# Kernel optimization log

Measured on AMD Instinct MI355X. Metric: run time of the kernel, lower is better.

Reference implementation:

```python
import jax, jax.numpy as jnp
import numpy as np

DIM, DEPTH, HEADS, DIM_HEAD, MLP = 768, 6, 12, 64, 3072
INNER = HEADS * DIM_HEAD
B, N = 8, 1024
SCALE = DIM_HEAD ** -0.5
EPS = 1e-5


def _ln(x, g, b):
    m = jnp.mean(x, -1, keepdims=True)
    v = jnp.mean(jnp.square(x - m), -1, keepdims=True)
    return (x - m) * jax.lax.rsqrt(v + EPS) * g + b


def _ternary(w):
    # BitNet-style ternary quant with straight-through estimator
    s = jnp.mean(jnp.abs(w)) + 1e-8
    wq = jnp.clip(jnp.round(w / s), -1.0, 1.0) * s
    return w + jax.lax.stop_gradient(wq - w)


def setup_inputs() -> dict:
    key = jax.random.key(0)
    ks = jax.random.split(key, 8)
    d = {
        'x': jax.random.normal(ks[0], (B, N, DIM), jnp.float32),
        'ln1_g': jnp.ones((DEPTH, DIM), jnp.float32),
        'ln1_b': jnp.zeros((DEPTH, DIM), jnp.float32),
        'Wqkv': jax.random.normal(ks[1], (DEPTH, 3 * INNER, DIM), jnp.float32) * 0.02,
        'ln2_g': jnp.ones((DEPTH, INNER), jnp.float32),
        'ln2_b': jnp.zeros((DEPTH, INNER), jnp.float32),
        'Wo': jax.random.normal(ks[2], (DEPTH, DIM, INNER), jnp.float32) * 0.02,
        'bo': jnp.zeros((DEPTH, DIM), jnp.float32),
        'ffln1_g': jnp.ones((DEPTH, DIM), jnp.float32),
        'ffln1_b': jnp.zeros((DEPTH, DIM), jnp.float32),
        'W1': jax.random.normal(ks[3], (DEPTH, MLP, DIM), jnp.float32) * 0.02,
        'b1': jnp.zeros((DEPTH, MLP), jnp.float32),
        'ffln2_g': jnp.ones((DEPTH, MLP), jnp.float32),
        'ffln2_b': jnp.zeros((DEPTH, MLP), jnp.float32),
        'W2': jax.random.normal(ks[4], (DEPTH, DIM, MLP), jnp.float32) * 0.02,
        'b2': jnp.zeros((DEPTH, DIM), jnp.float32),
    }
    return d


def _forward(x, ln1_g, ln1_b, Wqkv, ln2_g, ln2_b, Wo, bo,
             ffln1_g, ffln1_b, W1, b1, ffln2_g, ffln2_b, W2, b2):
    depth = Wqkv.shape[0]
    # layers 0..depth-2 ternary, last layer plain linear
    flag = jnp.concatenate([jnp.ones((depth - 1,), x.dtype), jnp.zeros((1,), x.dtype)])

    def block(h, p):
        (g1, b1n, wqkv, g2, b2n, wo, bo_, fg1, fb1, w1, bb1, fg2, fb2, w2, bb2, f) = p

        def mt(w):
            return f * _ternary(w) + (1.0 - f) * w

        y = _ln(h, g1, b1n)
        qkv = jnp.einsum('bnd,ed->bne', y, mt(wqkv))  # [B,N,3*INNER]
        q, k, v = jnp.split(qkv, 3, axis=-1)
        def heads(t):
            return t.reshape(B, N, HEADS, DIM_HEAD).transpose(0, 2, 1, 3)
        q, k, v = heads(q), heads(k), heads(v)
        attn = jax.nn.softmax(jnp.einsum('bhnd,bhmd->bhnm', q, k) * SCALE, axis=-1)
        o = jnp.einsum('bhnm,bhmd->bhnd', attn, v)
        o = o.transpose(0, 2, 1, 3).reshape(B, N, INNER)
        o = _ln(o, g2, b2n)
        o = jnp.einsum('bne,de->bnd', o, mt(wo)) + bo_
        h = h + o
        y = _ln(h, fg1, fb1)
        y = jnp.einsum('bnd,md->bnm', y, mt(w1)) + bb1
        y = jax.nn.gelu(y, approximate=False)
        y = _ln(y, fg2, fb2)
        y = jnp.einsum('bnm,dm->bnd', y, mt(w2)) + bb2
        return h + y, None

    xs = (ln1_g, ln1_b, Wqkv, ln2_g, ln2_b, Wo, bo,
          ffln1_g, ffln1_b, W1, b1, ffln2_g, ffln2_b, W2, b2, flag)
    out, _ = jax.lax.scan(block, x, xs)
    return out


def reference(x, ln1_g, ln1_b, Wqkv, ln2_g, ln2_b, Wo, bo,
              ffln1_g, ffln1_b, W1, b1, ffln2_g, ffln2_b, W2, b2):
    return _forward(x, ln1_g, ln1_b, Wqkv, ln2_g, ln2_b, Wo, bo,
                    ffln1_g, ffln1_b, W1, b1, ffln2_g, ffln2_b, W2, b2)
```

## Files before the change

kernel.cpp:

```cpp
#include <hip/hip_runtime.h>
#include <hip/hip_bf16.h>
#include <math.h>

typedef __bf16 bf16_t;
typedef __bf16 bf16x4 __attribute__((ext_vector_type(4)));
typedef __bf16 bf16x8 __attribute__((ext_vector_type(8)));
typedef float  f32x4  __attribute__((ext_vector_type(4)));

#define TOKENS 8192
#define DIMV   768
#define INNERV 768
#define QKVW   2304
#define MLPW   3072
#define NSEQ   1024
#define NB     8
#define NH     12
#define DH     64

enum { EP_STORE = 0, EP_BIAS_RES = 1, EP_BIAS_GELU = 2 };

__device__ __forceinline__ void gload_lds16(const bf16_t* g, bf16_t* l)
{
  __builtin_amdgcn_global_load_lds((const __attribute__((address_space(1))) void*)g,
                                   (__attribute__((address_space(3))) void*)l,
                                   16, 0, 0);
}

__device__ __forceinline__ float gelu_fast(float x)
{
  const float z = fabsf(x) * 0.70710678118654752f;
  const float d = fmaf(0.3275911f, z, 1.0f);
#if __has_builtin(__builtin_amdgcn_rcpf)
  const float t = __builtin_amdgcn_rcpf(d);
#else
  const float t = 1.0f / d;
#endif
  float p = fmaf(t, 1.061405429f, -1.453152027f);
  p = fmaf(t, p, 1.421413741f);
  p = fmaf(t, p, -0.284496736f);
  p = fmaf(t, p, 0.254829592f);
  p = t * p;
  const float e = __expf(-z * z);
  float erfv = fmaf(-p, e, 1.0f);
  erfv = copysignf(erfv, x);
  return 0.5f * x * (1.0f + erfv);
}

template <int BM>
__global__ __launch_bounds__(256)
void gemm_nt(const bf16_t* __restrict__ A, const bf16_t* __restrict__ B,
             const int K, const int N, const int mode,
             const float* __restrict__ sacc_p, const float sinvn, const float sbias,
             const float* __restrict__ bias,
             float* __restrict__ resid,
             bf16_t* __restrict__ outb,
             float* __restrict__ fout)
{
  constexpr int MI = BM / 32;
  constexpr int WR = BM / 2;
  __shared__ __align__(16) bf16_t lsA[2][BM * 32];
  __shared__ __align__(16) bf16_t lsB[2][128 * 32];
  const int tid  = threadIdx.x;
  const int lane = tid & 63;
  const int wave = tid >> 6;
  const int wm = wave >> 1, wn = wave & 1;
  const int bm = blockIdx.x, bn = blockIdx.y;

  const int srB   = wave * 32 + (lane >> 2);
  const int fswB  = (srB >> 1) & 3;
  const int scolB = ((lane & 3) ^ fswB) * 8;
  const bf16_t* gB = B + (size_t)(bn * 128 + srB) * K + scolB;
  const int lb0 = srB * 32 + (lane & 3) * 8;
  const int lb1 = (srB + 16) * 32 + (lane & 3) * 8;

  const int srA   = (BM == 128) ? srB : (wave * 16 + (lane >> 2));
  const int fswA  = (srA >> 1) & 3;
  const int scolA = ((lane & 3) ^ fswA) * 8;
  const bf16_t* gA = A + (size_t)(bm * BM + srA) * K + scolA;
  const int la0 = srA * 32 + (lane & 3) * 8;
  const int la1 = (srA + 16) * 32 + (lane & 3) * 8;

  f32x4 acc[MI][4];
#pragma unroll
  for (int i = 0; i < MI; i++)
#pragma unroll
    for (int j = 0; j < 4; j++) acc[i][j] = (f32x4){0.f, 0.f, 0.f, 0.f};

  const int fr   = ((lane & 15) >> 1) & 3;
  const int rsl  = ((lane >> 4) ^ fr) * 8;
  const int arow = (wm * WR + (lane & 15)) * 32 + rsl;
  const int brow = (wn * 64 + (lane & 15)) * 32 + rsl;

  auto stage = [&](int b, int kb) {
    gload_lds16(gA + kb, &lsA[b][la0]);
    if constexpr (BM == 128) gload_lds16(gA + (size_t)16 * K + kb, &lsA[b][la1]);
    gload_lds16(gB + kb, &lsB[b][lb0]);
    gload_lds16(gB + (size_t)16 * K + kb, &lsB[b][lb1]);
  };
  auto compute = [&](int b) {
    bf16x8 af[MI], bfv[4];
#pragma unroll
    for (int i = 0; i < MI; i++) af[i]  = *(const bf16x8*)&lsA[b][arow + i * 16 * 32];
#pragma unroll
    for (int j = 0; j < 4; j++)  bfv[j] = *(const bf16x8*)&lsB[b][brow + j * 16 * 32];
#pragma unroll
    for (int i = 0; i < MI; i++)
#pragma unroll
      for (int j = 0; j < 4; j++)
        acc[i][j] = __builtin_amdgcn_mfma_f32_16x16x32_bf16(af[i], bfv[j], acc[i][j], 0, 0, 0);
  };

  const int NT = K / 32;
  stage(0, 0);
  stage(1, 32);
  int cur = 0;
  for (int t = 0; t < NT - 1; ++t) {
    if constexpr (BM == 128) asm volatile("s_waitcnt vmcnt(4)" ::: "memory");
    else                     asm volatile("s_waitcnt vmcnt(3)" ::: "memory");
    __builtin_amdgcn_s_barrier();
    __builtin_amdgcn_sched_barrier(0);
    compute(cur);
    asm volatile("s_waitcnt lgkmcnt(0)" ::: "memory");
    __builtin_amdgcn_s_barrier();
    __builtin_amdgcn_sched_barrier(0);
    if (t + 2 < NT) stage(cur, (t + 2) * 32);
    cur ^= 1;
  }
  asm volatile("s_waitcnt vmcnt(0)" ::: "memory");
  __builtin_amdgcn_s_barrier();
  __builtin_amdgcn_sched_barrier(0);
  compute(cur);

  const float s = (*sacc_p) * sinvn + sbias;
  const int r0 = bm * BM + wm * WR + (lane >> 4) * 4;
  const int c0 = bn * 128 + wn * 64 + (lane & 15);
#pragma unroll
  for (int i = 0; i < MI; i++) {
#pragma unroll
    for (int j = 0; j < 4; j++) {
      const int col = c0 + j * 16;
#pragma unroll
      for (int r = 0; r < 4; r++) {
        const int row = r0 + i * 16 + r;
        const float v = acc[i][j][r] * s;
        const size_t idx = (size_t)row * N + col;
        if (mode == EP_STORE) {
          outb[idx] = (bf16_t)v;
        } else if (mode == EP_BIAS_RES) {
          const float add = v + bias[col];
          if (fout) fout[idx] = resid[idx] + add;
          else      resid[idx] += add;
        } else {
          outb[idx] = (bf16_t)gelu_fast(v + bias[col]);
        }
      }
    }
  }
}

template <typename TIN>
__global__ __launch_bounds__(256)
void ln_kern(const TIN* __restrict__ x, const float* __restrict__ g,
             const float* __restrict__ b, bf16_t* __restrict__ y, const int W)
{
  const int row = blockIdx.x;
  const int tid = threadIdx.x;
  const TIN* xr = x + (size_t)row * W;
  float s = 0.f, s2 = 0.f;
  if constexpr (sizeof(TIN) == 4) {
    const f32x4* xv = (const f32x4*)xr;
    for (int i = tid; i < W / 4; i += 256) {
      f32x4 v = xv[i];
#pragma unroll
      for (int e = 0; e < 4; e++) { s += v[e]; s2 += v[e] * v[e]; }
    }
  } else {
    const bf16x8* xv = (const bf16x8*)xr;
    for (int i = tid; i < W / 8; i += 256) {
      bf16x8 v = xv[i];
#pragma unroll
      for (int e = 0; e < 8; e++) { const float f = (float)v[e]; s += f; s2 += f * f; }
    }
  }
#pragma unroll
  for (int off = 32; off > 0; off >>= 1) {
    s  += __shfl_xor(s,  off, 64);
    s2 += __shfl_xor(s2, off, 64);
  }
  __shared__ float red[8];
  if ((tid & 63) == 0) { red[(tid >> 6) * 2] = s; red[(tid >> 6) * 2 + 1] = s2; }
  __syncthreads();
  const float ts  = red[0] + red[2] + red[4] + red[6];
  const float ts2 = red[1] + red[3] + red[5] + red[7];
  const float invW = 1.0f / (float)W;
  const float mean = ts * invW;
  const float var  = fmaxf(ts2 * invW - mean * mean, 0.f);
  const float rs   = rsqrtf(var + 1e-5f);
  bf16_t* yr = y + (size_t)row * W;
  const f32x4* gv = (const f32x4*)g;
  const f32x4* bv = (const f32x4*)b;
  if constexpr (sizeof(TIN) == 4) {
    const f32x4* xv = (const f32x4*)xr;
    bf16x4* yv = (bf16x4*)yr;
    for (int i = tid; i < W / 4; i += 256) {
      f32x4 v = xv[i], gg = gv[i], bb = bv[i];
      bf16x4 o;
#pragma unroll
      for (int e = 0; e < 4; e++) o[e] = (bf16_t)((v[e] - mean) * rs * gg[e] + bb[e]);
      yv[i] = o;
    }
  } else {
    const bf16x8* xv = (const bf16x8*)xr;
    bf16x8* yv = (bf16x8*)yr;
    for (int i = tid; i < W / 8; i += 256) {
      bf16x8 v = xv[i];
      f32x4 g0 = gv[2 * i], g1 = gv[2 * i + 1];
      f32x4 b0 = bv[2 * i], b1 = bv[2 * i + 1];
      bf16x8 o;
#pragma unroll
      for (int e = 0; e < 4; e++) o[e]     = (bf16_t)(((float)v[e]     - mean) * rs * g0[e] + b0[e]);
#pragma unroll
      for (int e = 0; e < 4; e++) o[e + 4] = (bf16_t)(((float)v[e + 4] - mean) * rs * g1[e] + b1[e]);
      yv[i] = o;
    }
  }
}

__global__ __launch_bounds__(256)
void attn_mfma(const bf16_t* __restrict__ qkv, bf16_t* __restrict__ o)
{
  __shared__ __align__(16) bf16_t Ks[64][72];
  __shared__ __align__(16) bf16_t Vt[64][72];
  __shared__ __align__(16) bf16_t Pw[4][16][72];
  const float SCL = 0.125f * 1.44269504088896f;
  const int tid  = threadIdx.x;
  const int lane = tid & 63;
  const int wave = tid >> 6;
  const int quad = lane >> 4;
  const int l15  = lane & 15;
  const int qb = blockIdx.x, hh = blockIdx.y, bb = blockIdx.z;
  const size_t tokbase = (size_t)bb * NSEQ;

  const int qrow = qb * 64 + wave * 16 + l15;
  bf16x8 qf[2];
  {
    const bf16_t* qp = qkv + (tokbase + qrow) * QKVW + hh * DH;
    qf[0] = *(const bf16x8*)(qp + quad * 8);
    qf[1] = *(const bf16x8*)(qp + 32 + quad * 8);
  }

  f32x4 Ot[4];
#pragma unroll
  for (int i = 0; i < 4; i++) Ot[i] = (f32x4){0.f, 0.f, 0.f, 0.f};
  float m2[4], lp[4];
#pragma unroll
  for (int r = 0; r < 4; r++) { m2[r] = -1e30f; lp[r] = 0.f; }

  const int skv = tid & 63;
  const int sd  = (tid >> 6) * 16;

  bf16x8 k0, k1, v0, v1;
  {
    const bf16_t* kp = qkv + (tokbase + skv) * QKVW + INNERV + hh * DH + sd;
    k0 = *(const bf16x8*)kp;
    k1 = *(const bf16x8*)(kp + 8);
    v0 = *(const bf16x8*)(kp + INNERV);
    v1 = *(const bf16x8*)(kp + INNERV + 8);
  }

  for (int kt = 0; kt < NSEQ / 64; ++kt) {
    __syncthreads();
    *(bf16x8*)&Ks[skv][sd]     = k0;
    *(bf16x8*)&Ks[skv][sd + 8] = k1;
#pragma unroll
    for (int e = 0; e < 8; e++) { Vt[sd + e][skv] = v0[e]; Vt[sd + 8 + e][skv] = v1[e]; }
    __syncthreads();

    bf16x8 nk0 = k0, nk1 = k1, nv0 = v0, nv1 = v1;
    if (kt + 1 < NSEQ / 64) {
      const bf16_t* kp = qkv + (tokbase + (kt + 1) * 64 + skv) * QKVW + INNERV + hh * DH + sd;
      nk0 = *(const bf16x8*)kp;
      nk1 = *(const bf16x8*)(kp + 8);
      nv0 = *(const bf16x8*)(kp + INNERV);
      nv1 = *(const bf16x8*)(kp + INNERV + 8);
    }

    f32x4 st[4];
    __builtin_amdgcn_s_setprio(1);
#pragma unroll
    for (int nt = 0; nt < 4; nt++) {
      bf16x8 b0 = *(const bf16x8*)&Ks[nt * 16 + l15][quad * 8];
      bf16x8 b1 = *(const bf16x8*)&Ks[nt * 16 + l15][32 + quad * 8];
      f32x4 c = (f32x4){0.f, 0.f, 0.f, 0.f};
      c = __builtin_amdgcn_mfma_f32_16x16x32_bf16(qf[0], b0, c, 0, 0, 0);
      c = __builtin_amdgcn_mfma_f32_16x16x32_bf16(qf[1], b1, c, 0, 0, 0);
      st[nt] = c;
    }
    __builtin_amdgcn_s_setprio(0);

    float rmax2[4];
#pragma unroll
    for (int r = 0; r < 4; r++) {
      float v = fmaxf(fmaxf(st[0][r], st[1][r]), fmaxf(st[2][r], st[3][r]));
      v = fmaxf(v, __shfl_xor(v, 1, 64));
      v = fmaxf(v, __shfl_xor(v, 2, 64));
      v = fmaxf(v, __shfl_xor(v, 4, 64));
      v = fmaxf(v, __shfl_xor(v, 8, 64));
      rmax2[r] = v * SCL;
    }
    const bool ok = (rmax2[0] <= m2[0] + 8.f) && (rmax2[1] <= m2[1] + 8.f) &&
                    (rmax2[2] <= m2[2] + 8.f) && (rmax2[3] <= m2[3] + 8.f);
    if (!__all(ok)) {
#pragma unroll
      for (int r = 0; r < 4; r++) {
        const float mnew = fmaxf(m2[r], rmax2[r]);
        const float alpha = exp2f(m2[r] - mnew);
        m2[r] = mnew;
        lp[r] *= alpha;
#pragma unroll
        for (int dt = 0; dt < 4; dt++) Ot[dt][r] *= alpha;
      }
    }
#pragma unroll
    for (int nt = 0; nt < 4; nt++) {
#pragma unroll
      for (int r = 0; r < 4; r++) {
        const float p = exp2f(fmaf(st[nt][r], SCL, -m2[r]));
        lp[r] += p;
        Pw[wave][quad * 4 + r][nt * 16 + l15] = (bf16_t)p;
      }
    }

    asm volatile("s_waitcnt lgkmcnt(0)" ::: "memory");
    __builtin_amdgcn_sched_barrier(0);

    __builtin_amdgcn_s_setprio(1);
#pragma unroll
    for (int kk = 0; kk < 2; kk++) {
      bf16x8 pa = *(const bf16x8*)&Pw[wave][l15][kk * 32 + quad * 8];
#pragma unroll
      for (int dt = 0; dt < 4; dt++) {
        bf16x8 vb = *(const bf16x8*)&Vt[dt * 16 + l15][kk * 32 + quad * 8];
        Ot[dt] = __builtin_amdgcn_mfma_f32_16x16x32_bf16(pa, vb, Ot[dt], 0, 0, 0);
      }
    }
    __builtin_amdgcn_s_setprio(0);

    k0 = nk0; k1 = nk1; v0 = nv0; v1 = nv1;
  }

  float inv[4];
#pragma unroll
  for (int r = 0; r < 4; r++) {
    float v = lp[r];
    v += __shfl_xor(v, 1, 64);
    v += __shfl_xor(v, 2, 64);
    v += __shfl_xor(v, 4, 64);
    v += __shfl_xor(v, 8, 64);
    inv[r] = 1.0f / v;
  }
#pragma unroll
  for (int dt = 0; dt < 4; dt++) {
#pragma unroll
    for (int r = 0; r < 4; r++) {
      const int q = qb * 64 + wave * 16 + quad * 4 + r;
      const int d = dt * 16 + l15;
      o[(tokbase + q) * INNERV + hh * DH + d] = (bf16_t)(Ot[dt][r] * inv[r]);
    }
  }
}

__global__ __launch_bounds__(64)
void zero_kern(float* __restrict__ p)
{
  p[threadIdx.x] = 0.f;
}

__global__ __launch_bounds__(256)
void absmean4_kern(const float* __restrict__ w0, const float* __restrict__ w1,
                   const float* __restrict__ w2, const float* __restrict__ w3,
                   const long n0, const long n1, const long n2, const long n3,
                   float* __restrict__ acc)
{
  const int t = blockIdx.y;
  const float* w = (t == 0) ? w0 : (t == 1) ? w1 : (t == 2) ? w2 : w3;
  const long  n  = (t == 0) ? n0 : (t == 1) ? n1 : (t == 2) ? n2 : n3;
  const int tid = threadIdx.x;
  float s = 0.f;
  const size_t stride = (size_t)256 * gridDim.x * 4;
  for (size_t i = ((size_t)blockIdx.x * 256 + tid) * 4; i < (size_t)n; i += stride) {
    f32x4 v = *(const f32x4*)(w + i);
    s += fabsf(v[0]) + fabsf(v[1]) + fabsf(v[2]) + fabsf(v[3]);
  }
#pragma unroll
  for (int off = 32; off > 0; off >>= 1) s += __shfl_xor(s, off, 64);
  __shared__ float red[4];
  if ((tid & 63) == 0) red[tid >> 6] = s;
  __syncthreads();
  if (tid == 0) atomicAdd(&acc[t], red[0] + red[1] + red[2] + red[3]);
}

__global__ __launch_bounds__(256)
void quant4_kern(const float* __restrict__ w0, const float* __restrict__ w1,
                 const float* __restrict__ w2, const float* __restrict__ w3,
                 bf16_t* __restrict__ q0, bf16_t* __restrict__ q1,
                 bf16_t* __restrict__ q2, bf16_t* __restrict__ q3,
                 const int n40, const int n41, const int n42, const int n43,
                 const float* __restrict__ acc,
                 const float inv0, const float inv1, const float inv2, const float inv3)
{
  const int t = blockIdx.y;
  const float* w = (t == 0) ? w0 : (t == 1) ? w1 : (t == 2) ? w2 : w3;
  bf16_t*      q = (t == 0) ? q0 : (t == 1) ? q1 : (t == 2) ? q2 : q3;
  const int   n4 = (t == 0) ? n40 : (t == 1) ? n41 : (t == 2) ? n42 : n43;
  const float iv = (t == 0) ? inv0 : (t == 1) ? inv1 : (t == 2) ? inv2 : inv3;
  const int i = blockIdx.x * 256 + threadIdx.x;
  if (i >= n4) return;
  const float s = acc[t] * iv + 1e-8f;
  f32x4 v = ((const f32x4*)w)[i];
  bf16x4 o;
#pragma unroll
  for (int e = 0; e < 4; e++) {
    float qv = rintf(v[e] / s);
    qv = fminf(1.f, fmaxf(-1.f, qv));
    o[e] = (bf16_t)qv;
  }
  ((bf16x4*)q)[i] = o;
}

__global__ __launch_bounds__(256)
void cast4_kern(const float* __restrict__ w0, const float* __restrict__ w1,
                const float* __restrict__ w2, const float* __restrict__ w3,
                bf16_t* __restrict__ q0, bf16_t* __restrict__ q1,
                bf16_t* __restrict__ q2, bf16_t* __restrict__ q3,
                const int n40, const int n41, const int n42, const int n43)
{
  const int t = blockIdx.y;
  const float* w = (t == 0) ? w0 : (t == 1) ? w1 : (t == 2) ? w2 : w3;
  bf16_t*      q = (t == 0) ? q0 : (t == 1) ? q1 : (t == 2) ? q2 : q3;
  const int   n4 = (t == 0) ? n40 : (t == 1) ? n41 : (t == 2) ? n42 : n43;
  const int i = blockIdx.x * 256 + threadIdx.x;
  if (i >= n4) return;
  f32x4 v = ((const f32x4*)w)[i];
  bf16x4 o;
#pragma unroll
  for (int e = 0; e < 4; e++) o[e] = (bf16_t)v[e];
  ((bf16x4*)q)[i] = o;
}

__global__ __launch_bounds__(256)
void copyf_kern(const float* __restrict__ in, float* __restrict__ out, const int n4)
{
  const int i = blockIdx.x * 256 + threadIdx.x;
  if (i < n4) ((f32x4*)out)[i] = ((const f32x4*)in)[i];
}

extern "C" void kernel_launch(void* const* d_in, const int* in_sizes, int n_in,
                              void* d_out, int out_size, void* d_ws, size_t ws_size,
                              hipStream_t stream)
{
  const float* x     = (const float*)d_in[0];
  const float* ln1_g = (const float*)d_in[1];
  const float* ln1_b = (const float*)d_in[2];
  const float* Wqkv  = (const float*)d_in[3];
  const float* ln2_g = (const float*)d_in[4];
  const float* ln2_b = (const float*)d_in[5];
  const float* Wo    = (const float*)d_in[6];
  const float* bo    = (const float*)d_in[7];
  const float* fg1   = (const float*)d_in[8];
  const float* fb1   = (const float*)d_in[9];
  const float* W1    = (const float*)d_in[10];
  const float* b1    = (const float*)d_in[11];
  const float* fg2   = (const float*)d_in[12];
  const float* fb2   = (const float*)d_in[13];
  const float* W2    = (const float*)d_in[14];
  const float* b2    = (const float*)d_in[15];

  char* ws = (char*)d_ws;
  size_t off = 0;
  float*  sacc  = (float*)(ws + off);  off += 256;
  float*  h     = (float*)(ws + off);  off += (size_t)TOKENS * DIMV * 4;
  bf16_t* bigA  = (bf16_t*)(ws + off); off += (size_t)TOKENS * MLPW * 2;
  bf16_t* bigB  = (bf16_t*)(ws + off); off += (size_t)TOKENS * MLPW * 2;
  bf16_t* q_qkv = (bf16_t*)(ws + off); off += (size_t)QKVW * DIMV * 2;
  bf16_t* q_o   = (bf16_t*)(ws + off); off += (size_t)DIMV * INNERV * 2;
  bf16_t* q_1   = (bf16_t*)(ws + off); off += (size_t)MLPW * DIMV * 2;
  bf16_t* q_2   = (bf16_t*)(ws + off); off += (size_t)DIMV * MLPW * 2;

  bf16_t* obuf   = bigA;
  bf16_t* ln2out = bigA + (size_t)TOKENS * INNERV;

  zero_kern<<<1, 64, 0, stream>>>(sacc);
  copyf_kern<<<TOKENS * DIMV / 4 / 256, 256, 0, stream>>>(x, h, TOKENS * DIMV / 4);

  for (int lyr = 0; lyr < 6; ++lyr) {
    const float* wqkv_l = Wqkv + (size_t)lyr * QKVW * DIMV;
    const float* wo_l   = Wo   + (size_t)lyr * DIMV * INNERV;
    const float* w1_l   = W1   + (size_t)lyr * MLPW * DIMV;
    const float* w2_l   = W2   + (size_t)lyr * DIMV * MLPW;
    const float *sq, *so, *s1, *s2p;
    float iq, io, i1, i2, bq, bo2, bb1v, bb2v;
    if (lyr < 5) {
      absmean4_kern<<<dim3(64, 4), 256, 0, stream>>>(
          wqkv_l, wo_l, w1_l, w2_l,
          (long)QKVW * DIMV, (long)DIMV * INNERV, (long)MLPW * DIMV, (long)DIMV * MLPW,
          &sacc[lyr * 4]);
      quant4_kern<<<dim3(MLPW * DIMV / 1024, 4), 256, 0, stream>>>(
          wqkv_l, wo_l, w1_l, w2_l, q_qkv, q_o, q_1, q_2,
          QKVW * DIMV / 4, DIMV * INNERV / 4, MLPW * DIMV / 4, DIMV * MLPW / 4,
          &sacc[lyr * 4],
          1.0f / (QKVW * DIMV), 1.0f / (DIMV * INNERV), 1.0f / (MLPW * DIMV), 1.0f / (DIMV * MLPW));
      sq = &sacc[lyr * 4 + 0]; iq = 1.0f / (QKVW * DIMV); bq = 1e-8f;
      so = &sacc[lyr * 4 + 1]; io = 1.0f / (DIMV * INNERV); bo2 = 1e-8f;
      s1 = &sacc[lyr * 4 + 2]; i1 = 1.0f / (MLPW * DIMV); bb1v = 1e-8f;
      s2p = &sacc[lyr * 4 + 3]; i2 = 1.0f / (DIMV * MLPW); bb2v = 1e-8f;
    } else {
      cast4_kern<<<dim3(MLPW * DIMV / 1024, 4), 256, 0, stream>>>(
          wqkv_l, wo_l, w1_l, w2_l, q_qkv, q_o, q_1, q_2,
          QKVW * DIMV / 4, DIMV * INNERV / 4, MLPW * DIMV / 4, DIMV * MLPW / 4);
      sq = so = s1 = s2p = &sacc[63];
      iq = io = i1 = i2 = 0.f;
      bq = bo2 = bb1v = bb2v = 1.0f;
    }

    ln_kern<float><<<TOKENS, 256, 0, stream>>>(h, ln1_g + lyr * DIMV, ln1_b + lyr * DIMV, bigA, DIMV);
    gemm_nt<128><<<dim3(64, QKVW / 128), 256, 0, stream>>>(bigA, q_qkv, DIMV, QKVW, EP_STORE, sq, iq, bq, nullptr, nullptr, bigB, nullptr);
    attn_mfma<<<dim3(NSEQ / 64, NH, NB), 256, 0, stream>>>(bigB, obuf);
    ln_kern<bf16_t><<<TOKENS, 256, 0, stream>>>(obuf, ln2_g + lyr * INNERV, ln2_b + lyr * INNERV, ln2out, INNERV);
    gemm_nt<64><<<dim3(TOKENS / 64, DIMV / 128), 256, 0, stream>>>(ln2out, q_o, INNERV, DIMV, EP_BIAS_RES, so, io, bo2, bo + lyr * DIMV, h, nullptr, nullptr);
    ln_kern<float><<<TOKENS, 256, 0, stream>>>(h, fg1 + lyr * DIMV, fb1 + lyr * DIMV, bigA, DIMV);
    gemm_nt<128><<<dim3(64, MLPW / 128), 256, 0, stream>>>(bigA, q_1, DIMV, MLPW, EP_BIAS_GELU, s1, i1, bb1v, b1 + lyr * MLPW, nullptr, bigB, nullptr);
    ln_kern<bf16_t><<<TOKENS, 256, 0, stream>>>(bigB, fg2 + lyr * MLPW, fb2 + lyr * MLPW, bigA, MLPW);
    gemm_nt<64><<<dim3(TOKENS / 64, DIMV / 128), 256, 0, stream>>>(bigA, q_2, MLPW, DIMV, EP_BIAS_RES, s2p, i2, bb2v, b2 + lyr * DIMV, h, nullptr,
                                                                   (lyr == 5) ? (float*)d_out : nullptr);
  }
}
```

Measured before the change: 2.408 ms.

## Triple-buffer GEMM LDS, defer attention row-max reduction, use exact GELU divide

The GEMM mainloop moves from two LDS buffers to three and drops the second barrier and lgkmcnt wait per K-step, so the next stage can be issued right after compute without waiting for every wave to finish reading. In attention, the cross-lane row-max shuffle reduction now runs only when some lane's local max exceeds the running max plus a threshold, which skips four shuffle rounds per row in the common case. GELU swaps the fast hardware reciprocal for an exact divide, which costs a little more ALU work. The extra LDS buffer raises shared memory per block and may lower occupancy. Removing the barrier relies on the three-buffer rotation to keep a wave from overwriting a buffer that a slower wave is still reading.

```diff
diff --git a/kernel.cpp b/kernel.cpp
--- a/kernel.cpp
+++ b/kernel.cpp
@@ -30,11 +30,7 @@
 {
   const float z = fabsf(x) * 0.70710678118654752f;
   const float d = fmaf(0.3275911f, z, 1.0f);
-#if __has_builtin(__builtin_amdgcn_rcpf)
-  const float t = __builtin_amdgcn_rcpf(d);
-#else
   const float t = 1.0f / d;
-#endif
   float p = fmaf(t, 1.061405429f, -1.453152027f);
   p = fmaf(t, p, 1.421413741f);
   p = fmaf(t, p, -0.284496736f);
@@ -58,8 +54,8 @@
 {
   constexpr int MI = BM / 32;
   constexpr int WR = BM / 2;
-  __shared__ __align__(16) bf16_t lsA[2][BM * 32];
-  __shared__ __align__(16) bf16_t lsB[2][128 * 32];
+  __shared__ __align__(16) bf16_t lsA[3][BM * 32];
+  __shared__ __align__(16) bf16_t lsB[3][128 * 32];
   const int tid  = threadIdx.x;
   const int lane = tid & 63;
   const int wave = tid >> 6;
@@ -113,23 +109,21 @@
   const int NT = K / 32;
   stage(0, 0);
   stage(1, 32);
-  int cur = 0;
+  int cb = 0, sb = 2;
   for (int t = 0; t < NT - 1; ++t) {
     if constexpr (BM == 128) asm volatile("s_waitcnt vmcnt(4)" ::: "memory");
     else                     asm volatile("s_waitcnt vmcnt(3)" ::: "memory");
     __builtin_amdgcn_s_barrier();
     __builtin_amdgcn_sched_barrier(0);
-    compute(cur);
-    asm volatile("s_waitcnt lgkmcnt(0)" ::: "memory");
-    __builtin_amdgcn_s_barrier();
-    __builtin_amdgcn_sched_barrier(0);
-    if (t + 2 < NT) stage(cur, (t + 2) * 32);
-    cur ^= 1;
+    compute(cb);
+    if (t + 2 < NT) stage(sb, (t + 2) * 32);
+    cb = (cb == 2) ? 0 : cb + 1;
+    sb = (sb == 2) ? 0 : sb + 1;
   }
   asm volatile("s_waitcnt vmcnt(0)" ::: "memory");
   __builtin_amdgcn_s_barrier();
   __builtin_amdgcn_sched_barrier(0);
-  compute(cur);
+  compute(cb);
 
   const float s = (*sacc_p) * sinvn + sbias;
   const int r0 = bm * BM + wm * WR + (lane >> 4) * 4;
@@ -298,22 +292,22 @@
     }
     __builtin_amdgcn_s_setprio(0);
 
-    float rmax2[4];
-#pragma unroll
-    for (int r = 0; r < 4; r++) {
-      float v = fmaxf(fmaxf(st[0][r], st[1][r]), fmaxf(st[2][r], st[3][r]));
-      v = fmaxf(v, __shfl_xor(v, 1, 64));
-      v = fmaxf(v, __shfl_xor(v, 2, 64));
-      v = fmaxf(v, __shfl_xor(v, 4, 64));
-      v = fmaxf(v, __shfl_xor(v, 8, 64));
-      rmax2[r] = v * SCL;
-    }
-    const bool ok = (rmax2[0] <= m2[0] + 8.f) && (rmax2[1] <= m2[1] + 8.f) &&
-                    (rmax2[2] <= m2[2] + 8.f) && (rmax2[3] <= m2[3] + 8.f);
+    float lm[4];
+#pragma unroll
+    for (int r = 0; r < 4; r++)
+      lm[r] = fmaxf(fmaxf(st[0][r], st[1][r]), fmaxf(st[2][r], st[3][r]));
+    const bool ok = (lm[0] * SCL <= m2[0] + 8.f) && (lm[1] * SCL <= m2[1] + 8.f) &&
+                    (lm[2] * SCL <= m2[2] + 8.f) && (lm[3] * SCL <= m2[3] + 8.f);
     if (!__all(ok)) {
 #pragma unroll
       for (int r = 0; r < 4; r++) {
-        const float mnew = fmaxf(m2[r], rmax2[r]);
+        float v = lm[r];
+        v = fmaxf(v, __shfl_xor(v, 1, 64));
+        v = fmaxf(v, __shfl_xor(v, 2, 64));
+        v = fmaxf(v, __shfl_xor(v, 4, 64));
+        v = fmaxf(v, __shfl_xor(v, 8, 64));
+        const float rmax2 = v * SCL;
+        const float mnew = fmaxf(m2[r], rmax2);
         const float alpha = exp2f(m2[r] - mnew);
         m2[r] = mnew;
         lp[r] *= alpha;
```

Result: faster. 2.343 ms (-2.7%).
